# Kernel optimization log

Hardware: AMD Instinct MI355X
Metric: run time of the kernel (lower is better)

## Reference

```python
import jax, jax.numpy as jnp
import numpy as np

NV, NC = 100000, 50000        # num variables, num constraints
DV, DC = 8, 16                # padded neighbor-list widths
DIN, DH = 32, 128             # init_input_dim, output_dim (=init_output_dim)
NUM_LAYERS = 3                # aggregate loop runs num_layers-1 times
DCAT = 2 * DH + DIN           # input_dim of fc_variable/fc_constraint


def setup_inputs() -> dict:
    key = jax.random.key(0)
    ks = jax.random.split(key, 10)
    w = lambda k, shape: (jax.random.normal(k, shape, jnp.float32) * 0.05)
    return {
        "x": jax.random.normal(ks[0], (NV + NC, DIN), jnp.float32),
        "var_constr_index": jax.random.randint(ks[1], (NV, DV), 0, NC, dtype=jnp.int32),
        "constr_var_index": jax.random.randint(ks[2], (NC, DC), 0, NV, dtype=jnp.int32),
        "W_init_v": w(ks[3], (DIN, DH)), "b_init_v": jnp.zeros((DH,), jnp.float32),
        "W_init_c": w(ks[4], (DIN, DH)), "b_init_c": jnp.zeros((DH,), jnp.float32),
        "W_var": w(ks[5], (DCAT, DH)), "b_var": jnp.zeros((DH,), jnp.float32),
        "W_con": w(ks[6], (DCAT, DH)), "b_con": jnp.zeros((DH,), jnp.float32),
        "W_q": w(ks[7], (2 * DH, 1)), "b_q": jnp.zeros((1,), jnp.float32),
    }


def reference(x, var_constr_index, constr_var_index,
              W_init_v, b_init_v, W_init_c, b_init_c,
              W_var, b_var, W_con, b_con, W_q, b_q):
    nv = var_constr_index.shape[0]
    xv, xc = x[:nv], x[nv:]
    # layer zero init (fc_init_variables / fc_init_constraints)
    v = xv @ W_init_v + b_init_v          # [NV, DH]
    c = xc @ W_init_c + b_init_c          # [NC, DH]
    # message-passing layers: both updates read OLD v and OLD c
    for _ in range(1, NUM_LAYERS):
        agg_c = jnp.sum(v[constr_var_index], axis=1)   # [NC, DH] gather+sum over variable neighbors
        agg_v = jnp.sum(c[var_constr_index], axis=1)   # [NV, DH] gather+sum over constraint neighbors
        c_new = jnp.concatenate([agg_c, c, xc], axis=1) @ W_con + b_con
        v_new = jnp.concatenate([agg_v, v, xv], axis=1) @ W_var + b_var
        c, v = c_new, v_new
    # embedding_Q: global sum of variable features, broadcast, concat, linear
    g = jnp.sum(v, axis=0)                             # [DH]
    q_in = jnp.concatenate([jnp.broadcast_to(g, v.shape), v], axis=1)  # [NV, 2*DH]
    return q_in @ W_q + b_q                            # [NV, 1]
```

## Files before the change

### kernel.cpp

```cpp
#include <hip/hip_runtime.h>

#define NV 100000
#define NC 50000
#define DVAR 8
#define DCON 16

using short8 = __attribute__((ext_vector_type(8))) short;
using f32x4  = __attribute__((ext_vector_type(4))) float;

__device__ __forceinline__ unsigned short f2bf(float f) {
    union { float f; unsigned int u; } v; v.f = f;
    return (unsigned short)((v.u + 0x7fffu + ((v.u >> 16) & 1u)) >> 16);
}
__device__ __forceinline__ float bflo(unsigned int u) {
    union { unsigned int u; float f; } v; v.u = u << 16; return v.f;
}
__device__ __forceinline__ float bfhi(unsigned int u) {
    union { unsigned int u; float f; } v; v.u = u & 0xffff0000u; return v.f;
}

__global__ __launch_bounds__(256) void pack_kernel(
    const float* __restrict__ Wvar, const float* __restrict__ Wcon,
    const float* __restrict__ Wiv,  const float* __restrict__ Wic,
    unsigned short* __restrict__ WbVar, unsigned short* __restrict__ WbCon,
    unsigned short* __restrict__ WbIv,  unsigned short* __restrict__ WbIc,
    float* __restrict__ S)
{
    const int tid = blockIdx.x * 256 + threadIdx.x;
    for (int i = tid; i < 9 * 128 * 32; i += gridDim.x * 256) {
        int s = i >> 12, rem = i & 4095, c = rem >> 5, k = rem & 31;
        int src = (s * 32 + k) * 128 + c;
        WbVar[i] = f2bf(Wvar[src]);
        WbCon[i] = f2bf(Wcon[src]);
    }
    for (int i = tid; i < 128 * 32; i += gridDim.x * 256) {
        int c = i >> 5, k = i & 31;
        int src = k * 128 + c;
        WbIv[i] = f2bf(Wiv[src]);
        WbIc[i] = f2bf(Wic[src]);
    }
    if (tid == 0) S[0] = 0.f;
}

__global__ __launch_bounds__(256) void init_mfma(
    const float* __restrict__ x,
    const unsigned short* __restrict__ Wb,
    const float* __restrict__ bias,
    unsigned short* __restrict__ hout, int M)
{
    const int t = threadIdx.x;
    const int lane = t & 63;
    const int w = t >> 6;
    const int lrow = lane & 15;
    const int lg = lane >> 4;
    const int wrow0 = blockIdx.x * 64 + w * 16;
    int arow = wrow0 + lrow;
    int arowc = arow < M ? arow : M - 1;

    const float4* xp = (const float4*)(x + (size_t)arowc * 32 + lg * 8);
    float4 xa = xp[0], xb = xp[1];
    short8 afr;
    afr[0] = (short)f2bf(xa.x); afr[1] = (short)f2bf(xa.y);
    afr[2] = (short)f2bf(xa.z); afr[3] = (short)f2bf(xa.w);
    afr[4] = (short)f2bf(xb.x); afr[5] = (short)f2bf(xb.y);
    afr[6] = (short)f2bf(xb.z); afr[7] = (short)f2bf(xb.w);

    #pragma unroll
    for (int ct = 0; ct < 8; ++ct) {
        int c = ct * 16 + lrow;
        short8 bfr = *(const short8*)(Wb + (size_t)c * 32 + lg * 8);
        f32x4 acc = {0.f, 0.f, 0.f, 0.f};
        acc = __builtin_amdgcn_mfma_f32_16x16x32_bf16(afr, bfr, acc, 0, 0, 0);
        float bv = bias[c];
        #pragma unroll
        for (int r = 0; r < 4; ++r) {
            int orow = wrow0 + lg * 4 + r;
            if (orow < M) hout[(size_t)orow * 128 + c] = f2bf(acc[r] + bv);
        }
    }
}

template<int DEG>
__global__ __launch_bounds__(256) void agg_bf16(
    const unsigned short* __restrict__ hnb, const int* __restrict__ idx,
    unsigned short* __restrict__ agg, int M)
{
    const int tid = blockIdx.x * 256 + threadIdx.x;
    const int row = tid >> 4;
    const int part = tid & 15;
    if (row >= M) return;
    int nb[DEG];
    #pragma unroll
    for (int d4 = 0; d4 < DEG / 4; ++d4)
        *(int4*)(&nb[d4 * 4]) = *(const int4*)(idx + (size_t)row * DEG + d4 * 4);
    float a0=0.f,a1=0.f,a2=0.f,a3=0.f,a4=0.f,a5=0.f,a6=0.f,a7=0.f;
    #pragma unroll
    for (int b = 0; b < DEG; b += 8) {
        uint4 q[8];
        #pragma unroll
        for (int j = 0; j < 8; ++j)
            q[j] = *(const uint4*)(hnb + (size_t)nb[b + j] * 128 + part * 8);
        #pragma unroll
        for (int j = 0; j < 8; ++j) {
            a0 += bflo(q[j].x); a1 += bfhi(q[j].x);
            a2 += bflo(q[j].y); a3 += bfhi(q[j].y);
            a4 += bflo(q[j].z); a5 += bfhi(q[j].z);
            a6 += bflo(q[j].w); a7 += bfhi(q[j].w);
        }
    }
    uint4 o;
    o.x = (unsigned)f2bf(a0) | ((unsigned)f2bf(a1) << 16);
    o.y = (unsigned)f2bf(a2) | ((unsigned)f2bf(a3) << 16);
    o.z = (unsigned)f2bf(a4) | ((unsigned)f2bf(a5) << 16);
    o.w = (unsigned)f2bf(a6) | ((unsigned)f2bf(a7) << 16);
    *(uint4*)(agg + (size_t)row * 128 + part * 8) = o;
}

template<bool FINAL>
__global__ __launch_bounds__(256) void gemm_mfma(
    const unsigned short* hself,
    const unsigned short* __restrict__ aggin,
    const float* __restrict__ xself,
    const unsigned short* __restrict__ Wb,
    const float* __restrict__ bias,
    unsigned short* hout,
    const float* __restrict__ Wq, float* __restrict__ S, float* __restrict__ dotout,
    int M)
{
    __shared__ float red[4];
    const int t = threadIdx.x;
    const int lane = t & 63;
    const int w = t >> 6;
    const int lrow = lane & 15;
    const int lg = lane >> 4;
    const int wrow0 = blockIdx.x * 64 + w * 16;
    const int arow = wrow0 + lrow;
    const int arowc = arow < M ? arow : M - 1;

    short8 afr[9];
    #pragma unroll
    for (int s = 0; s < 4; ++s)
        afr[s] = *(const short8*)(aggin + (size_t)arowc * 128 + s * 32 + lg * 8);
    #pragma unroll
    for (int s = 0; s < 4; ++s)
        afr[4 + s] = *(const short8*)(hself + (size_t)arowc * 128 + s * 32 + lg * 8);
    {
        const float4* xp = (const float4*)(xself + (size_t)arowc * 32 + lg * 8);
        float4 xa = xp[0], xb = xp[1];
        short8 xfr;
        xfr[0] = (short)f2bf(xa.x); xfr[1] = (short)f2bf(xa.y);
        xfr[2] = (short)f2bf(xa.z); xfr[3] = (short)f2bf(xa.w);
        xfr[4] = (short)f2bf(xb.x); xfr[5] = (short)f2bf(xb.y);
        xfr[6] = (short)f2bf(xb.z); xfr[7] = (short)f2bf(xb.w);
        afr[8] = xfr;
    }

    f32x4 acc[8];
    #pragma unroll
    for (int ct = 0; ct < 8; ++ct) acc[ct] = (f32x4){0.f, 0.f, 0.f, 0.f};

    #pragma unroll
    for (int s = 0; s < 9; ++s) {
        #pragma unroll
        for (int ct = 0; ct < 8; ++ct) {
            short8 bfr = *(const short8*)(Wb + ((size_t)s * 128 + ct * 16 + lrow) * 32 + lg * 8);
            acc[ct] = __builtin_amdgcn_mfma_f32_16x16x32_bf16(afr[s], bfr, acc[ct], 0, 0, 0);
        }
    }

    if (!FINAL) {
        #pragma unroll
        for (int ct = 0; ct < 8; ++ct) {
            int c = ct * 16 + lrow;
            float bv = bias[c];
            #pragma unroll
            for (int r = 0; r < 4; ++r) {
                int orow = wrow0 + lg * 4 + r;
                if (orow < M) hout[(size_t)orow * 128 + c] = f2bf(acc[ct][r] + bv);
            }
        }
    } else {
        float d0[4] = {0.f, 0.f, 0.f, 0.f};
        float d1[4] = {0.f, 0.f, 0.f, 0.f};
        #pragma unroll
        for (int ct = 0; ct < 8; ++ct) {
            int c = ct * 16 + lrow;
            float bv = bias[c];
            float wq0 = Wq[c];
            float wq1 = Wq[128 + c];
            #pragma unroll
            for (int r = 0; r < 4; ++r) {
                int orow = wrow0 + lg * 4 + r;
                float val = (orow < M) ? (acc[ct][r] + bv) : 0.f;
                d0[r] += val * wq0;
                d1[r] += val * wq1;
            }
        }
        #pragma unroll
        for (int r = 0; r < 4; ++r) {
            d0[r] += __shfl_xor(d0[r], 1); d0[r] += __shfl_xor(d0[r], 2);
            d0[r] += __shfl_xor(d0[r], 4); d0[r] += __shfl_xor(d0[r], 8);
            d1[r] += __shfl_xor(d1[r], 1); d1[r] += __shfl_xor(d1[r], 2);
            d1[r] += __shfl_xor(d1[r], 4); d1[r] += __shfl_xor(d1[r], 8);
        }
        if (lrow == 0) {
            #pragma unroll
            for (int r = 0; r < 4; ++r) {
                int orow = wrow0 + lg * 4 + r;
                if (orow < M) dotout[orow] = d1[r];
            }
        }
        float tot = d0[0] + d0[1] + d0[2] + d0[3];
        tot += __shfl_xor(tot, 16);
        tot += __shfl_xor(tot, 32);
        if (lane == 0) red[w] = tot;
        __syncthreads();
        if (t == 0) atomicAdd(S, red[0] + red[1] + red[2] + red[3]);
    }
}

__global__ __launch_bounds__(256) void addout_kernel(
    float* __restrict__ outp, const float* __restrict__ S,
    const float* __restrict__ bq, int n)
{
    int i = blockIdx.x * 256 + threadIdx.x;
    if (i < n) outp[i] = outp[i] + S[0] + bq[0];
}

extern "C" void kernel_launch(void* const* d_in, const int* in_sizes, int n_in,
                              void* d_out, int out_size, void* d_ws, size_t ws_size,
                              hipStream_t stream)
{
    const float* x    = (const float*)d_in[0];
    const int*   vci  = (const int*)  d_in[1];
    const int*   cvi  = (const int*)  d_in[2];
    const float* Wiv  = (const float*)d_in[3];
    const float* biv  = (const float*)d_in[4];
    const float* Wic  = (const float*)d_in[5];
    const float* bic  = (const float*)d_in[6];
    const float* Wvar = (const float*)d_in[7];
    const float* bvar = (const float*)d_in[8];
    const float* Wcon = (const float*)d_in[9];
    const float* bcon = (const float*)d_in[10];
    const float* Wq   = (const float*)d_in[11];
    const float* bq   = (const float*)d_in[12];
    float* outp = (float*)d_out;

    unsigned short* us = (unsigned short*)d_ws;
    size_t o = 0;
    unsigned short* vA    = us + o; o += (size_t)NV * 128;
    unsigned short* cA    = us + o; o += (size_t)NC * 128;
    unsigned short* cB    = us + o; o += (size_t)NC * 128;
    unsigned short* aggV  = us + o; o += (size_t)NV * 128;
    unsigned short* aggC  = us + o; o += (size_t)NC * 128;
    unsigned short* WbVar = us + o; o += 9 * 128 * 32;
    unsigned short* WbCon = us + o; o += 9 * 128 * 32;
    unsigned short* WbIv  = us + o; o += 128 * 32;
    unsigned short* WbIc  = us + o; o += 128 * 32;
    float* S = (float*)(us + o);

    const float* xc = x + (size_t)NV * 32;

    pack_kernel<<<144, 256, 0, stream>>>(Wvar, Wcon, Wiv, Wic, WbVar, WbCon, WbIv, WbIc, S);
    init_mfma<<<(NV + 63) / 64, 256, 0, stream>>>(x,  WbIv, biv, vA, NV);
    init_mfma<<<(NC + 63) / 64, 256, 0, stream>>>(xc, WbIc, bic, cA, NC);

    agg_bf16<DCON><<<(NC * 16 + 255) / 256, 256, 0, stream>>>(vA, cvi, aggC, NC);
    agg_bf16<DVAR><<<(NV * 16 + 255) / 256, 256, 0, stream>>>(cA, vci, aggV, NV);
    gemm_mfma<false><<<(NC + 63) / 64, 256, 0, stream>>>(
        cA, aggC, xc, WbCon, bcon, cB, nullptr, nullptr, nullptr, NC);
    gemm_mfma<false><<<(NV + 63) / 64, 256, 0, stream>>>(
        vA, aggV, x, WbVar, bvar, vA, nullptr, nullptr, nullptr, NV);

    agg_bf16<DVAR><<<(NV * 16 + 255) / 256, 256, 0, stream>>>(cB, vci, aggV, NV);
    gemm_mfma<true><<<(NV + 63) / 64, 256, 0, stream>>>(
        vA, aggV, x, WbVar, bvar, nullptr, Wq, S, outp, NV);

    addout_kernel<<<(NV + 255) / 256, 256, 0, stream>>>(outp, S, bq, NV);
}
```

Measured before the change: 303.7 us.

## Process two row tiles per wave and double-buffer A/B fragment loads in gemm

Each wave now computes 32 rows (two 16-row MFMA tiles) instead of 16, so every B (weight) fragment loaded from global memory is reused for two MFMAs and the grid is halved. The K loop also prefetches the next step's A and B fragments into a second register buffer while the current step's MFMAs issue, overlapping load latency with compute. The cost is roughly double the accumulator and fragment registers, which may lower occupancy, and fewer blocks to spread across CUs.

New measurement: 297.3 us. 2.1% less time.

```diff
diff --git a/kernel.cpp b/kernel.cpp
--- a/kernel.cpp
+++ b/kernel.cpp
@@ -133,84 +133,114 @@
     const int w = t >> 6;
     const int lrow = lane & 15;
     const int lg = lane >> 4;
-    const int wrow0 = blockIdx.x * 64 + w * 16;
-    const int arow = wrow0 + lrow;
-    const int arowc = arow < M ? arow : M - 1;
-
-    short8 afr[9];
-    #pragma unroll
-    for (int s = 0; s < 4; ++s)
-        afr[s] = *(const short8*)(aggin + (size_t)arowc * 128 + s * 32 + lg * 8);
-    #pragma unroll
-    for (int s = 0; s < 4; ++s)
-        afr[4 + s] = *(const short8*)(hself + (size_t)arowc * 128 + s * 32 + lg * 8);
-    {
-        const float4* xp = (const float4*)(xself + (size_t)arowc * 32 + lg * 8);
-        float4 xa = xp[0], xb = xp[1];
-        short8 xfr;
-        xfr[0] = (short)f2bf(xa.x); xfr[1] = (short)f2bf(xa.y);
-        xfr[2] = (short)f2bf(xa.z); xfr[3] = (short)f2bf(xa.w);
-        xfr[4] = (short)f2bf(xb.x); xfr[5] = (short)f2bf(xb.y);
-        xfr[6] = (short)f2bf(xb.z); xfr[7] = (short)f2bf(xb.w);
-        afr[8] = xfr;
-    }
-
-    f32x4 acc[8];
-    #pragma unroll
-    for (int ct = 0; ct < 8; ++ct) acc[ct] = (f32x4){0.f, 0.f, 0.f, 0.f};
+    const int wrow0 = blockIdx.x * 128 + w * 32;
+
+    int arc[2];
+    #pragma unroll
+    for (int rt = 0; rt < 2; ++rt) {
+        int r = wrow0 + rt * 16 + lrow;
+        arc[rt] = r < M ? r : M - 1;
+    }
+
+    auto loadA = [&](int s, int rt) -> short8 {
+        if (s < 4) {
+            return *(const short8*)(aggin + (size_t)arc[rt] * 128 + s * 32 + lg * 8);
+        } else if (s < 8) {
+            return *(const short8*)(hself + (size_t)arc[rt] * 128 + (s - 4) * 32 + lg * 8);
+        } else {
+            const float4* xp = (const float4*)(xself + (size_t)arc[rt] * 32 + lg * 8);
+            float4 xa = xp[0], xb = xp[1];
+            short8 r8;
+            r8[0] = (short)f2bf(xa.x); r8[1] = (short)f2bf(xa.y);
+            r8[2] = (short)f2bf(xa.z); r8[3] = (short)f2bf(xa.w);
+            r8[4] = (short)f2bf(xb.x); r8[5] = (short)f2bf(xb.y);
+            r8[6] = (short)f2bf(xb.z); r8[7] = (short)f2bf(xb.w);
+            return r8;
+        }
+    };
+
+    short8 bfr[2][8];
+    short8 afr[2][2];
+    #pragma unroll
+    for (int ct = 0; ct < 8; ++ct)
+        bfr[0][ct] = *(const short8*)(Wb + ((size_t)(ct * 16 + lrow)) * 32 + lg * 8);
+    afr[0][0] = loadA(0, 0);
+    afr[0][1] = loadA(0, 1);
+
+    f32x4 acc[2][8];
+    #pragma unroll
+    for (int rt = 0; rt < 2; ++rt)
+        #pragma unroll
+        for (int ct = 0; ct < 8; ++ct) acc[rt][ct] = (f32x4){0.f, 0.f, 0.f, 0.f};
 
     #pragma unroll
     for (int s = 0; s < 9; ++s) {
-        #pragma unroll
-        for (int ct = 0; ct < 8; ++ct) {
-            short8 bfr = *(const short8*)(Wb + ((size_t)s * 128 + ct * 16 + lrow) * 32 + lg * 8);
-            acc[ct] = __builtin_amdgcn_mfma_f32_16x16x32_bf16(afr[s], bfr, acc[ct], 0, 0, 0);
-        }
+        const int cur = s & 1, nxt = cur ^ 1;
+        if (s < 8) {
+            #pragma unroll
+            for (int ct = 0; ct < 8; ++ct)
+                bfr[nxt][ct] = *(const short8*)(
+                    Wb + ((size_t)(s + 1) * 128 + ct * 16 + lrow) * 32 + lg * 8);
+            afr[nxt][0] = loadA(s + 1, 0);
+            afr[nxt][1] = loadA(s + 1, 1);
+        }
+        #pragma unroll
+        for (int ct = 0; ct < 8; ++ct)
+            #pragma unroll
+            for (int rt = 0; rt < 2; ++rt)
+                acc[rt][ct] = __builtin_amdgcn_mfma_f32_16x16x32_bf16(
+                    afr[cur][rt], bfr[cur][ct], acc[rt][ct], 0, 0, 0);
     }
 
     if (!FINAL) {
         #pragma unroll
-        for (int ct = 0; ct < 8; ++ct) {
-            int c = ct * 16 + lrow;
-            float bv = bias[c];
+        for (int rt = 0; rt < 2; ++rt)
+            #pragma unroll
+            for (int ct = 0; ct < 8; ++ct) {
+                int c = ct * 16 + lrow;
+                float bv = bias[c];
+                #pragma unroll
+                for (int r = 0; r < 4; ++r) {
+                    int orow = wrow0 + rt * 16 + lg * 4 + r;
+                    if (orow < M) hout[(size_t)orow * 128 + c] = f2bf(acc[rt][ct][r] + bv);
+                }
+            }
+    } else {
+        float tot = 0.f;
+        #pragma unroll
+        for (int rt = 0; rt < 2; ++rt) {
+            float d0[4] = {0.f, 0.f, 0.f, 0.f};
+            float d1[4] = {0.f, 0.f, 0.f, 0.f};
+            #pragma unroll
+            for (int ct = 0; ct < 8; ++ct) {
+                int c = ct * 16 + lrow;
+                float bv = bias[c];
+                float wq0 = Wq[c];
+                float wq1 = Wq[128 + c];
+                #pragma unroll
+                for (int r = 0; r < 4; ++r) {
+                    int orow = wrow0 + rt * 16 + lg * 4 + r;
+                    float val = (orow < M) ? (acc[rt][ct][r] + bv) : 0.f;
+                    d0[r] += val * wq0;
+                    d1[r] += val * wq1;
+                }
+            }
             #pragma unroll
             for (int r = 0; r < 4; ++r) {
-                int orow = wrow0 + lg * 4 + r;
-                if (orow < M) hout[(size_t)orow * 128 + c] = f2bf(acc[ct][r] + bv);
+                d0[r] += __shfl_xor(d0[r], 1); d0[r] += __shfl_xor(d0[r], 2);
+                d0[r] += __shfl_xor(d0[r], 4); d0[r] += __shfl_xor(d0[r], 8);
+                d1[r] += __shfl_xor(d1[r], 1); d1[r] += __shfl_xor(d1[r], 2);
+                d1[r] += __shfl_xor(d1[r], 4); d1[r] += __shfl_xor(d1[r], 8);
             }
-        }
-    } else {
-        float d0[4] = {0.f, 0.f, 0.f, 0.f};
-        float d1[4] = {0.f, 0.f, 0.f, 0.f};
-        #pragma unroll
-        for (int ct = 0; ct < 8; ++ct) {
-            int c = ct * 16 + lrow;
-            float bv = bias[c];
-            float wq0 = Wq[c];
-            float wq1 = Wq[128 + c];
-            #pragma unroll
-            for (int r = 0; r < 4; ++r) {
-                int orow = wrow0 + lg * 4 + r;
-                float val = (orow < M) ? (acc[ct][r] + bv) : 0.f;
-                d0[r] += val * wq0;
-                d1[r] += val * wq1;
+            if (lrow == 0) {
+                #pragma unroll
+                for (int r = 0; r < 4; ++r) {
+                    int orow = wrow0 + rt * 16 + lg * 4 + r;
+                    if (orow < M) dotout[orow] = d1[r];
+                }
             }
-        }
-        #pragma unroll
-        for (int r = 0; r < 4; ++r) {
-            d0[r] += __shfl_xor(d0[r], 1); d0[r] += __shfl_xor(d0[r], 2);
-            d0[r] += __shfl_xor(d0[r], 4); d0[r] += __shfl_xor(d0[r], 8);
-            d1[r] += __shfl_xor(d1[r], 1); d1[r] += __shfl_xor(d1[r], 2);
-            d1[r] += __shfl_xor(d1[r], 4); d1[r] += __shfl_xor(d1[r], 8);
-        }
-        if (lrow == 0) {
-            #pragma unroll
-            for (int r = 0; r < 4; ++r) {
-                int orow = wrow0 + lg * 4 + r;
-                if (orow < M) dotout[orow] = d1[r];
-            }
-        }
-        float tot = d0[0] + d0[1] + d0[2] + d0[3];
+            tot += d0[0] + d0[1] + d0[2] + d0[3];
+        }
         tot += __shfl_xor(tot, 16);
         tot += __shfl_xor(tot, 32);
         if (lane == 0) red[w] = tot;
@@ -267,13 +297,13 @@
 
     agg_bf16<DCON><<<(NC * 16 + 255) / 256, 256, 0, stream>>>(vA, cvi, aggC, NC);
     agg_bf16<DVAR><<<(NV * 16 + 255) / 256, 256, 0, stream>>>(cA, vci, aggV, NV);
-    gemm_mfma<false><<<(NC + 63) / 64, 256, 0, stream>>>(
+    gemm_mfma<false><<<(NC + 127) / 128, 256, 0, stream>>>(
         cA, aggC, xc, WbCon, bcon, cB, nullptr, nullptr, nullptr, NC);
-    gemm_mfma<false><<<(NV + 63) / 64, 256, 0, stream>>>(
+    gemm_mfma<false><<<(NV + 127) / 128, 256, 0, stream>>>(
         vA, aggV, x, WbVar, bvar, vA, nullptr, nullptr, nullptr, NV);
 
     agg_bf16<DVAR><<<(NV * 16 + 255) / 256, 256, 0, stream>>>(cB, vci, aggV, NV);
-    gemm_mfma<true><<<(NV + 63) / 64, 256, 0, stream>>>(
+    gemm_mfma<true><<<(NV + 127) / 128, 256, 0, stream>>>(
         vA, aggV, x, WbVar, bvar, nullptr, Wq, S, outp, NV);
 
     addout_kernel<<<(NV + 255) / 256, 256, 0, stream>>>(outp, S, bq, NV);
```

## Stage GEMM A tiles in LDS via async global_load_lds and double-buffer B fragments

Applied to the files above, without the earlier changes.

The GEMM kernel now copies the 64-row agg and self-feature tiles into swizzled shared memory with global_load_lds, so the loads are coalesced across whole rows instead of each lane fetching strided fragments. It then reads A fragments from LDS and prefetches the next step's weight fragments into a double buffer to overlap loads with MFMA work. Launch bounds request two blocks per SM. This adds 32KB of LDS per block and extra register pressure, which may limit occupancy.

Result: no change. 298.3 us (-1.8%).

```diff
diff --git a/kernel.cpp b/kernel.cpp
--- a/kernel.cpp
+++ b/kernel.cpp
@@ -7,6 +7,9 @@
 
 using short8 = __attribute__((ext_vector_type(8))) short;
 using f32x4  = __attribute__((ext_vector_type(4))) float;
+
+typedef const __attribute__((address_space(1))) void* as1cv;
+typedef __attribute__((address_space(3))) void* as3v;
 
 __device__ __forceinline__ unsigned short f2bf(float f) {
     union { float f; unsigned int u; } v; v.f = f;
@@ -117,7 +120,7 @@
 }
 
 template<bool FINAL>
-__global__ __launch_bounds__(256) void gemm_mfma(
+__global__ __launch_bounds__(256, 2) void gemm_mfma(
     const unsigned short* hself,
     const unsigned short* __restrict__ aggin,
     const float* __restrict__ xself,
@@ -127,45 +130,78 @@
     const float* __restrict__ Wq, float* __restrict__ S, float* __restrict__ dotout,
     int M)
 {
+    __shared__ __align__(16) unsigned short Aagg[64 * 128];
+    __shared__ __align__(16) unsigned short Aself[64 * 128];
     __shared__ float red[4];
     const int t = threadIdx.x;
     const int lane = t & 63;
     const int w = t >> 6;
     const int lrow = lane & 15;
     const int lg = lane >> 4;
-    const int wrow0 = blockIdx.x * 64 + w * 16;
+    const int r0 = blockIdx.x * 64;
+    const int wrow0 = r0 + w * 16;
     const int arow = wrow0 + lrow;
     const int arowc = arow < M ? arow : M - 1;
 
-    short8 afr[9];
-    #pragma unroll
-    for (int s = 0; s < 4; ++s)
-        afr[s] = *(const short8*)(aggin + (size_t)arowc * 128 + s * 32 + lg * 8);
-    #pragma unroll
-    for (int s = 0; s < 4; ++s)
-        afr[4 + s] = *(const short8*)(hself + (size_t)arowc * 128 + s * 32 + lg * 8);
+    short8 xfr;
     {
         const float4* xp = (const float4*)(xself + (size_t)arowc * 32 + lg * 8);
         float4 xa = xp[0], xb = xp[1];
-        short8 xfr;
         xfr[0] = (short)f2bf(xa.x); xfr[1] = (short)f2bf(xa.y);
         xfr[2] = (short)f2bf(xa.z); xfr[3] = (short)f2bf(xa.w);
         xfr[4] = (short)f2bf(xb.x); xfr[5] = (short)f2bf(xb.y);
         xfr[6] = (short)f2bf(xb.z); xfr[7] = (short)f2bf(xb.w);
-        afr[8] = xfr;
-    }
+    }
+
+    #pragma unroll
+    for (int i = 0; i < 4; ++i) {
+        int L = i * 256 + t;
+        int row = L >> 4, c = L & 15;
+        int gr = r0 + row;
+        int grc = gr < M ? gr : M - 1;
+        int cs = c ^ (row & 7);
+        __builtin_amdgcn_global_load_lds(
+            (as1cv)(aggin + (size_t)grc * 128 + cs * 8),
+            (as3v)(&Aagg[(size_t)L * 8]), 16, 0, 0);
+        __builtin_amdgcn_global_load_lds(
+            (as1cv)(hself + (size_t)grc * 128 + cs * 8),
+            (as3v)(&Aself[(size_t)L * 8]), 16, 0, 0);
+    }
+
+    short8 bfr[2][8];
+    #pragma unroll
+    for (int ct = 0; ct < 8; ++ct)
+        bfr[0][ct] = *(const short8*)(Wb + (size_t)(ct * 16 + lrow) * 32 + lg * 8);
+
+    __syncthreads();
+
+    auto ldsA = [&](const unsigned short* base, int srel) -> short8 {
+        int chunk = (4 * srel + lg) ^ (lrow & 7);
+        return *(const short8*)(base + ((size_t)(w * 16 + lrow) * 16 + chunk) * 8);
+    };
 
     f32x4 acc[8];
     #pragma unroll
     for (int ct = 0; ct < 8; ++ct) acc[ct] = (f32x4){0.f, 0.f, 0.f, 0.f};
 
+    short8 afr = ldsA(Aagg, 0);
     #pragma unroll
     for (int s = 0; s < 9; ++s) {
-        #pragma unroll
-        for (int ct = 0; ct < 8; ++ct) {
-            short8 bfr = *(const short8*)(Wb + ((size_t)s * 128 + ct * 16 + lrow) * 32 + lg * 8);
-            acc[ct] = __builtin_amdgcn_mfma_f32_16x16x32_bf16(afr[s], bfr, acc[ct], 0, 0, 0);
-        }
+        const int cur = s & 1, nxt = cur ^ 1;
+        short8 afr_nxt;
+        if (s < 8) {
+            #pragma unroll
+            for (int ct = 0; ct < 8; ++ct)
+                bfr[nxt][ct] = *(const short8*)(
+                    Wb + ((size_t)(s + 1) * 128 + ct * 16 + lrow) * 32 + lg * 8);
+            afr_nxt = (s + 1 < 4) ? ldsA(Aagg, s + 1)
+                    : (s + 1 < 8) ? ldsA(Aself, s + 1 - 4)
+                                  : xfr;
+        }
+        #pragma unroll
+        for (int ct = 0; ct < 8; ++ct)
+            acc[ct] = __builtin_amdgcn_mfma_f32_16x16x32_bf16(afr, bfr[cur][ct], acc[ct], 0, 0, 0);
+        afr = afr_nxt;
     }
 
     if (!FINAL) {
```
